# Kernel optimization log

Measured on AMD Instinct MI355X. Metric: run time of the kernel, lower is better.

Reference implementation:

```python
import jax, jax.numpy as jnp
import numpy as np

EPS = 1e-5  # torch LayerNorm default

def _ln(x, w, b):
    mu = jnp.mean(x, axis=-1, keepdims=True)
    var = jnp.mean((x - mu) ** 2, axis=-1, keepdims=True)
    return (x - mu) * jax.lax.rsqrt(var + EPS) * w + b

def setup_inputs() -> dict:
    B, C, P, D = 256, 256, 256, 256  # broadcasting in final add requires B==P==C
    key = jax.random.key(0)
    ks = jax.random.split(key, 10)
    d_rsqrt = D ** -0.5
    return {
        "x": jax.random.normal(ks[0], (B, C), dtype=jnp.float32),
        "prev_cell_out": jax.random.normal(ks[1], (P, D), dtype=jnp.float32),
        "feature_emb_weight": jax.random.uniform(ks[2], (C, D), minval=-d_rsqrt, maxval=d_rsqrt),
        "feature_emb_bias": jax.random.uniform(ks[3], (1, C, D), minval=-d_rsqrt, maxval=d_rsqrt),
        "ln_emb_w": jnp.ones((D,), jnp.float32), "ln_emb_b": jnp.zeros((D,), jnp.float32),
        "ln_col_w": jnp.ones((D,), jnp.float32), "ln_col_b": jnp.zeros((D,), jnp.float32),
        "ln_prompt_w": jnp.ones((D,), jnp.float32), "ln_prompt_b": jnp.zeros((D,), jnp.float32),
        "dense_imp_w": jax.random.normal(ks[4], (D, 2 * D)) * (2 * D) ** -0.5,  # torch Linear weight [out,in]
        "dense_imp_b": jnp.zeros((D,), jnp.float32),
        "emb_column": jax.random.normal(ks[5], (C, D)) * 0.01,
        "emb_prompt": jax.random.normal(ks[6], (P, D)) * 0.01,
        "expand_weight": jax.random.normal(ks[7], (P, 1)),  # dense_expand.weight [n_prompts, 1]
        "expand_bias": jax.random.normal(ks[8], (P,)) * 0.01,
    }

def reference(x, prev_cell_out, feature_emb_weight, feature_emb_bias,
              ln_emb_w, ln_emb_b, ln_col_w, ln_col_b, ln_prompt_w, ln_prompt_b,
              dense_imp_w, dense_imp_b, emb_column, emb_prompt,
              expand_weight, expand_bias):
    # addcmul: bias + x[...,None] * weight -> [B, C, D]
    x_emb = _ln(jax.nn.relu(feature_emb_bias + x[..., None] * feature_emb_weight), ln_emb_w, ln_emb_b)
    # prompt path (unbatched): [P, 2D] -> [P, D]
    xp_in = jnp.concatenate([_ln(emb_prompt, ln_prompt_w, ln_prompt_b), prev_cell_out], axis=-1)
    x_prompt = xp_in @ dense_imp_w.T + dense_imp_b + emb_prompt
    x_col = _ln(emb_column, ln_col_w, ln_col_b)  # [C, D]
    mask = jax.nn.softmax(x_prompt @ x_col.T, axis=-1)  # [P, C]
    # einsum 'pc,bcd->bpd'
    x_out = jnp.einsum('pc,bcd->bpd', mask, x_emb)
    # 'pc,bcd,pa->bpd' with a==1 is the same contraction scaled per-prompt by expand_weight[p,0]
    x_out = x_out * (1.0 + expand_weight[:, 0])[None, :, None]
    # 'pc,p->pc' then unsqueeze(0).unsqueeze(-1): [1, P, C, 1]; broadcasts [B,P,D] -> [1,B,P,D]
    bias_term = (mask * expand_bias[:, None])[None, :, :, None]
    return x_out + bias_term  # [1, B, P, D] (B==P==C)
```

## Files before the change

kernel.cpp:

```cpp
#include <hip/hip_runtime.h>
#include <cstdint>

typedef _Float16 half8 __attribute__((ext_vector_type(8)));
typedef float f32x4 __attribute__((ext_vector_type(4)));

#define LN_EPS 1e-5f

__device__ __forceinline__ float dot4(float4 a, float4 b) {
  return a.x*b.x + a.y*b.y + a.z*b.z + a.w*b.w;
}

__global__ __launch_bounds__(256) void k_pre(
    const float* __restrict__ x, const float* __restrict__ few, const float* __restrict__ feb,
    const float* __restrict__ emb_pr, const float* __restrict__ lnp_w, const float* __restrict__ lnp_b,
    const float* __restrict__ prev, const float* __restrict__ W, const float* __restrict__ Wb,
    const float* __restrict__ emb_col, const float* __restrict__ lnc_w, const float* __restrict__ lnc_b,
    float2* __restrict__ stats2, float* __restrict__ mask_f32, _Float16* __restrict__ mask_f16)
{
  __shared__ __align__(16) struct {
    float xin[512];
    float xq[256];
    float sc[256];
    float wr1[4], wr2[4];
  } sm;

  int t = threadIdx.x, w = t >> 6, lane = t & 63;

  if (blockIdx.x >= 256) {
    int bid = blockIdx.x - 256;
    int b = bid >> 3;
    int cg = (bid & 7) * 4 + w;
    int c0 = cg * 8;
    float xv[8];
    #pragma unroll
    for (int j = 0; j < 8; ++j) xv[j] = x[b*256 + c0 + j];
    float s1[8], s2[8];
    #pragma unroll
    for (int j = 0; j < 8; ++j) { s1[j] = 0.f; s2[j] = 0.f; }
    #pragma unroll
    for (int j = 0; j < 8; ++j) {
      float4 fw = ((const float4*)few)[(c0+j)*64 + lane];
      float4 fb = ((const float4*)feb)[(c0+j)*64 + lane];
      float4 v;
      v.x = fmaxf(fb.x + xv[j]*fw.x, 0.f);
      v.y = fmaxf(fb.y + xv[j]*fw.y, 0.f);
      v.z = fmaxf(fb.z + xv[j]*fw.z, 0.f);
      v.w = fmaxf(fb.w + xv[j]*fw.w, 0.f);
      s1[j] += v.x + v.y + v.z + v.w;
      s2[j] += v.x*v.x + v.y*v.y + v.z*v.z + v.w*v.w;
    }
    #pragma unroll
    for (int o = 32; o > 0; o >>= 1) {
      #pragma unroll
      for (int j = 0; j < 8; ++j) { s1[j] += __shfl_xor(s1[j], o); s2[j] += __shfl_xor(s2[j], o); }
    }
    float mu[8], rs[8];
    #pragma unroll
    for (int j = 0; j < 8; ++j) {
      mu[j] = s1[j] * (1.0f/256.0f);
      float var = s2[j] * (1.0f/256.0f) - mu[j]*mu[j];
      rs[j] = rsqrtf(var + LN_EPS);
    }
    float muv = mu[0], rsv = rs[0];
    #pragma unroll
    for (int j = 1; j < 8; ++j) {
      muv = (lane == j) ? mu[j] : muv;
      rsv = (lane == j) ? rs[j] : rsv;
    }
    if (lane < 8) stats2[b*256 + c0 + lane] = make_float2(muv, rsv);
    return;
  }

  int p = blockIdx.x;
  int q = t & 3, g = t >> 2;

  {
    float4 v = ((const float4*)emb_pr)[p*64 + lane];
    float s1 = v.x + v.y + v.z + v.w;
    float s2 = v.x*v.x + v.y*v.y + v.z*v.z + v.w*v.w;
    #pragma unroll
    for (int o = 32; o > 0; o >>= 1) { s1 += __shfl_xor(s1, o); s2 += __shfl_xor(s2, o); }
    float mu = s1 * (1.0f/256.0f);
    float var = s2 * (1.0f/256.0f) - mu*mu;
    float rsv = rsqrtf(var + LN_EPS);
    float4 w4 = ((const float4*)lnp_w)[lane];
    float4 b4 = ((const float4*)lnp_b)[lane];
    float4 y;
    y.x = (v.x-mu)*rsv*w4.x + b4.x;  y.y = (v.y-mu)*rsv*w4.y + b4.y;
    y.z = (v.z-mu)*rsv*w4.z + b4.z;  y.w = (v.w-mu)*rsv*w4.w + b4.w;
    if (w == 0) {
      ((float4*)sm.xin)[lane] = y;
      ((float4*)sm.xin)[64 + lane] = ((const float4*)prev)[p*64 + lane];
    }
  }
  __syncthreads();

  {
    float acc[4] = {0.f, 0.f, 0.f, 0.f};
    #pragma unroll 4
    for (int j = 0; j < 32; ++j) {
      int k4 = j*4 + q;
      float4 xv = ((const float4*)sm.xin)[k4];
      #pragma unroll
      for (int pp = 0; pp < 4; ++pp) {
        int d = pp*64 + g;
        float4 wv = ((const float4*)W)[d*128 + k4];
        acc[pp] += dot4(wv, xv);
      }
    }
    #pragma unroll
    for (int pp = 0; pp < 4; ++pp) {
      acc[pp] += __shfl_xor(acc[pp], 1);
      acc[pp] += __shfl_xor(acc[pp], 2);
    }
    if (q == 0) {
      #pragma unroll
      for (int pp = 0; pp < 4; ++pp) {
        int d = pp*64 + g;
        sm.xq[d] = acc[pp] + Wb[d] + emb_pr[p*256 + d];
      }
    }
  }
  __syncthreads();

  {
    float s1[4] = {0,0,0,0}, s2[4] = {0,0,0,0};
    #pragma unroll 4
    for (int j = 0; j < 16; ++j) {
      int k4 = j*4 + q;
      #pragma unroll
      for (int pp = 0; pp < 4; ++pp) {
        float4 v = ((const float4*)emb_col)[(pp*64+g)*64 + k4];
        s1[pp] += v.x + v.y + v.z + v.w;
        s2[pp] += v.x*v.x + v.y*v.y + v.z*v.z + v.w*v.w;
      }
    }
    float mu[4], rs[4];
    #pragma unroll
    for (int pp = 0; pp < 4; ++pp) {
      s1[pp] += __shfl_xor(s1[pp], 1);  s1[pp] += __shfl_xor(s1[pp], 2);
      s2[pp] += __shfl_xor(s2[pp], 1);  s2[pp] += __shfl_xor(s2[pp], 2);
      mu[pp] = s1[pp] * (1.0f/256.0f);
      float var = s2[pp] * (1.0f/256.0f) - mu[pp]*mu[pp];
      rs[pp] = rsqrtf(var + LN_EPS);
    }
    float acc[4] = {0.f, 0.f, 0.f, 0.f};
    #pragma unroll 4
    for (int j = 0; j < 16; ++j) {
      int k4 = j*4 + q;
      float4 lw4 = ((const float4*)lnc_w)[k4];
      float4 lb4 = ((const float4*)lnc_b)[k4];
      float4 xv = ((const float4*)sm.xq)[k4];
      #pragma unroll
      for (int pp = 0; pp < 4; ++pp) {
        float4 v = ((const float4*)emb_col)[(pp*64+g)*64 + k4];
        float4 nc;
        nc.x = (v.x-mu[pp])*rs[pp]*lw4.x + lb4.x;
        nc.y = (v.y-mu[pp])*rs[pp]*lw4.y + lb4.y;
        nc.z = (v.z-mu[pp])*rs[pp]*lw4.z + lb4.z;
        nc.w = (v.w-mu[pp])*rs[pp]*lw4.w + lb4.w;
        acc[pp] += dot4(nc, xv);
      }
    }
    #pragma unroll
    for (int pp = 0; pp < 4; ++pp) {
      acc[pp] += __shfl_xor(acc[pp], 1);
      acc[pp] += __shfl_xor(acc[pp], 2);
    }
    if (q == 0) {
      #pragma unroll
      for (int pp = 0; pp < 4; ++pp) sm.sc[pp*64 + g] = acc[pp];
    }
  }
  __syncthreads();

  {
    float val = sm.sc[t];
    float m0 = val;
    #pragma unroll
    for (int o = 32; o > 0; o >>= 1) m0 = fmaxf(m0, __shfl_xor(m0, o));
    if (lane == 0) sm.wr1[w] = m0;
    __syncthreads();
    float M = fmaxf(fmaxf(sm.wr1[0], sm.wr1[1]), fmaxf(sm.wr1[2], sm.wr1[3]));
    float e = expf(val - M);
    float s = e;
    #pragma unroll
    for (int o = 32; o > 0; o >>= 1) s += __shfl_xor(s, o);
    if (lane == 0) sm.wr2[w] = s;
    __syncthreads();
    float S = sm.wr2[0] + sm.wr2[1] + sm.wr2[2] + sm.wr2[3];
    float mv = e / S;
    mask_f32[p*256 + t] = mv;
    mask_f16[p*256 + t] = (_Float16)mv;
  }
}

__global__ __launch_bounds__(256) void k_main(
    const float* __restrict__ x, const float* __restrict__ few, const float* __restrict__ feb,
    const float* __restrict__ ln_emb_w, const float* __restrict__ ln_emb_b,
    const float2* __restrict__ stats2,
    const _Float16* __restrict__ mask_f16, const float* __restrict__ mask_f32,
    const float* __restrict__ ew, const float* __restrict__ eb,
    float* __restrict__ out)
{
  __shared__ __align__(16) _Float16 Bs[2][8 * 64 * 8];
  __shared__ float xrow[256];
  __shared__ __align__(8) float2 srow[256];

  const int t = threadIdx.x, w = t >> 6, lane = t & 63;
  const int lm = lane & 15, quad = lane >> 4;
  const int b  = blockIdx.x >> 2;
  const int ds = (blockIdx.x & 3) * 64;
  const int dl = t & 63;
  const int d  = ds + dl;

  half8 mf[2][4];
  #pragma unroll
  for (int ks = 0; ks < 2; ++ks)
    #pragma unroll
    for (int nt = 0; nt < 4; ++nt)
      mf[ks][nt] = *(const half8*)(mask_f16 + (size_t)(w*64 + nt*16 + lm)*256 + ks*32 + quad*8);

  xrow[t] = x[b*256 + t];
  srow[t] = stats2[b*256 + t];
  const float lwv = ln_emb_w[d];
  const float lbv = ln_emb_b[d];

  f32x4 acc[4][4];
  #pragma unroll
  for (int i = 0; i < 4; ++i)
    #pragma unroll
    for (int j = 0; j < 4; ++j)
      acc[i][j] = (f32x4){0.f, 0.f, 0.f, 0.f};

  float fwv[16], fbv[16];
  #pragma unroll
  for (int j = 0; j < 16; ++j) {
    int cl = w*16 + j;
    fwv[j] = few[cl*256 + d];
    fbv[j] = feb[cl*256 + d];
  }
  __syncthreads();
  {
    half8 h0, h1;
    #pragma unroll
    for (int j = 0; j < 16; ++j) {
      int cl = w*16 + j;
      float2 st = srow[cl];
      float v = fmaxf(fbv[j] + xrow[cl]*fwv[j], 0.f);
      _Float16 hh = (_Float16)((v - st.x) * st.y * lwv + lbv);
      if (j < 8) h0[j] = hh; else h1[j-8] = hh;
    }
    *(half8*)(&Bs[0][((w*2 + 0)*64 + dl)*8]) = h0;
    *(half8*)(&Bs[0][((w*2 + 1)*64 + dl)*8]) = h1;
  }
  __syncthreads();

  #pragma unroll
  for (int kb = 0; kb < 4; ++kb) {
    if (kb < 3) {
      #pragma unroll
      for (int j = 0; j < 16; ++j) {
        int cl = (kb+1)*64 + w*16 + j;
        fwv[j] = few[cl*256 + d];
        fbv[j] = feb[cl*256 + d];
      }
    }
    const _Float16* Bcur = &Bs[kb & 1][0];
    #pragma unroll
    for (int ks = 0; ks < 2; ++ks) {
      half8 xf[4];
      #pragma unroll
      for (int mt = 0; mt < 4; ++mt)
        xf[mt] = *(const half8*)(Bcur + ((ks*4 + quad)*64 + mt*16 + lm)*8);
      #pragma unroll
      for (int mt = 0; mt < 4; ++mt)
        #pragma unroll
        for (int nt = 0; nt < 4; ++nt)
          acc[mt][nt] = __builtin_amdgcn_mfma_f32_16x16x32_f16(xf[mt], mf[ks][nt], acc[mt][nt], 0, 0, 0);
    }
    if (kb < 3) {
      #pragma unroll
      for (int ks = 0; ks < 2; ++ks)
        #pragma unroll
        for (int nt = 0; nt < 4; ++nt)
          mf[ks][nt] = *(const half8*)(mask_f16 + (size_t)(w*64 + nt*16 + lm)*256 + (kb+1)*64 + ks*32 + quad*8);
      half8 h0, h1;
      #pragma unroll
      for (int j = 0; j < 16; ++j) {
        int cl = (kb+1)*64 + w*16 + j;
        float2 st = srow[cl];
        float v = fmaxf(fbv[j] + xrow[cl]*fwv[j], 0.f);
        _Float16 hh = (_Float16)((v - st.x) * st.y * lwv + lbv);
        if (j < 8) h0[j] = hh; else h1[j-8] = hh;
      }
      *(half8*)(&Bs[(kb+1) & 1][((w*2 + 0)*64 + dl)*8]) = h0;
      *(half8*)(&Bs[(kb+1) & 1][((w*2 + 1)*64 + dl)*8]) = h1;
      __syncthreads();
    }
  }

  const float ebv = eb[b];
  float sp[4], tb[4];
  #pragma unroll
  for (int nt = 0; nt < 4; ++nt) {
    int p = w*64 + nt*16 + lm;
    sp[nt] = 1.0f + ew[p];
    tb[nt] = mask_f32[b*256 + p] * ebv;
  }
  #pragma unroll
  for (int mt = 0; mt < 4; ++mt) {
    #pragma unroll
    for (int nt = 0; nt < 4; ++nt) {
      int p = w*64 + nt*16 + lm;
      int dd = ds + mt*16 + quad*4;
      f32x4 o = acc[mt][nt] * sp[nt] + tb[nt];
      *(f32x4*)(out + ((size_t)b << 16) + ((size_t)p << 8) + dd) = o;
    }
  }
}

extern "C" void kernel_launch(void* const* d_in, const int* in_sizes, int n_in,
                              void* d_out, int out_size, void* d_ws, size_t ws_size,
                              hipStream_t stream) {
  const float* x        = (const float*)d_in[0];
  const float* prev     = (const float*)d_in[1];
  const float* few      = (const float*)d_in[2];
  const float* feb      = (const float*)d_in[3];
  const float* ln_emb_w = (const float*)d_in[4];
  const float* ln_emb_b = (const float*)d_in[5];
  const float* ln_col_w = (const float*)d_in[6];
  const float* ln_col_b = (const float*)d_in[7];
  const float* ln_pr_w  = (const float*)d_in[8];
  const float* ln_pr_b  = (const float*)d_in[9];
  const float* dimp_w   = (const float*)d_in[10];
  const float* dimp_b   = (const float*)d_in[11];
  const float* emb_col  = (const float*)d_in[12];
  const float* emb_pr   = (const float*)d_in[13];
  const float* ew       = (const float*)d_in[14];
  const float* eb       = (const float*)d_in[15];
  float* out = (float*)d_out;

  char* wsb = (char*)d_ws;
  float2*   ws_stats  = (float2*)(wsb);
  float*    ws_mask   = (float*)(wsb + 524288);
  _Float16* ws_mask_h = (_Float16*)(wsb + 786432);

  k_pre<<<dim3(256 + 2048), dim3(256), 0, stream>>>(
      x, few, feb,
      emb_pr, ln_pr_w, ln_pr_b, prev, dimp_w, dimp_b,
      emb_col, ln_col_w, ln_col_b,
      ws_stats, ws_mask, ws_mask_h);
  k_main<<<dim3(1024), dim3(256), 0, stream>>>(
      x, few, feb, ln_emb_w, ln_emb_b,
      ws_stats, ws_mask_h, ws_mask, ew, eb, out);
}
```

Before: 148.1 us.

## Stage all embedding K-blocks in LDS upfront, then run MFMA with register-prefetched mask

The interleaved double-buffered pipeline is replaced by two phases. First, all four K-blocks of the LayerNorm'd embedding tile are computed and written to a larger LDS buffer behind a single barrier. Then the MFMA loop runs with no barriers, ping-ponging mask fragments between two register sets so the next block's mask load is issued before the current block's MFMAs. This removes three block-wide syncs, at the cost of more LDS (32KB for Bs), extra registers, and no overlap between the embedding compute and the MFMAs.

```diff
diff --git a/kernel.cpp b/kernel.cpp
--- a/kernel.cpp
+++ b/kernel.cpp
@@ -203,7 +203,7 @@
     const float* __restrict__ ew, const float* __restrict__ eb,
     float* __restrict__ out)
 {
-  __shared__ __align__(16) _Float16 Bs[2][8 * 64 * 8];
+  __shared__ __align__(16) _Float16 Bs[4 * 8 * 64 * 8];
   __shared__ float xrow[256];
   __shared__ __align__(8) float2 srow[256];
 
@@ -214,12 +214,12 @@
   const int dl = t & 63;
   const int d  = ds + dl;
 
-  half8 mf[2][4];
+  half8 mf0[2][4], mf1[2][4];
   #pragma unroll
   for (int ks = 0; ks < 2; ++ks)
     #pragma unroll
     for (int nt = 0; nt < 4; ++nt)
-      mf[ks][nt] = *(const half8*)(mask_f16 + (size_t)(w*64 + nt*16 + lm)*256 + ks*32 + quad*8);
+      mf0[ks][nt] = *(const half8*)(mask_f16 + (size_t)(w*64 + nt*16 + lm)*256 + ks*32 + quad*8);
 
   xrow[t] = x[b*256 + t];
   srow[t] = stats2[b*256 + t];
@@ -233,72 +233,55 @@
     for (int j = 0; j < 4; ++j)
       acc[i][j] = (f32x4){0.f, 0.f, 0.f, 0.f};
 
-  float fwv[16], fbv[16];
-  #pragma unroll
-  for (int j = 0; j < 16; ++j) {
-    int cl = w*16 + j;
-    fwv[j] = few[cl*256 + d];
-    fbv[j] = feb[cl*256 + d];
-  }
-  __syncthreads();
-  {
+  __syncthreads();
+
+  #pragma unroll
+  for (int kb = 0; kb < 4; ++kb) {
+    float fwv[16], fbv[16];
+    #pragma unroll
+    for (int j = 0; j < 16; ++j) {
+      int cl = kb*64 + w*16 + j;
+      fwv[j] = few[cl*256 + d];
+      fbv[j] = feb[cl*256 + d];
+    }
     half8 h0, h1;
     #pragma unroll
     for (int j = 0; j < 16; ++j) {
-      int cl = w*16 + j;
+      int cl = kb*64 + w*16 + j;
       float2 st = srow[cl];
       float v = fmaxf(fbv[j] + xrow[cl]*fwv[j], 0.f);
       _Float16 hh = (_Float16)((v - st.x) * st.y * lwv + lbv);
       if (j < 8) h0[j] = hh; else h1[j-8] = hh;
     }
-    *(half8*)(&Bs[0][((w*2 + 0)*64 + dl)*8]) = h0;
-    *(half8*)(&Bs[0][((w*2 + 1)*64 + dl)*8]) = h1;
-  }
-  __syncthreads();
-
-  #pragma unroll
-  for (int kb = 0; kb < 4; ++kb) {
-    if (kb < 3) {
-      #pragma unroll
-      for (int j = 0; j < 16; ++j) {
-        int cl = (kb+1)*64 + w*16 + j;
-        fwv[j] = few[cl*256 + d];
-        fbv[j] = feb[cl*256 + d];
-      }
-    }
-    const _Float16* Bcur = &Bs[kb & 1][0];
-    #pragma unroll
-    for (int ks = 0; ks < 2; ++ks) {
-      half8 xf[4];
-      #pragma unroll
-      for (int mt = 0; mt < 4; ++mt)
-        xf[mt] = *(const half8*)(Bcur + ((ks*4 + quad)*64 + mt*16 + lm)*8);
-      #pragma unroll
-      for (int mt = 0; mt < 4; ++mt)
-        #pragma unroll
-        for (int nt = 0; nt < 4; ++nt)
-          acc[mt][nt] = __builtin_amdgcn_mfma_f32_16x16x32_f16(xf[mt], mf[ks][nt], acc[mt][nt], 0, 0, 0);
-    }
-    if (kb < 3) {
-      #pragma unroll
-      for (int ks = 0; ks < 2; ++ks)
-        #pragma unroll
-        for (int nt = 0; nt < 4; ++nt)
-          mf[ks][nt] = *(const half8*)(mask_f16 + (size_t)(w*64 + nt*16 + lm)*256 + (kb+1)*64 + ks*32 + quad*8);
-      half8 h0, h1;
-      #pragma unroll
-      for (int j = 0; j < 16; ++j) {
-        int cl = (kb+1)*64 + w*16 + j;
-        float2 st = srow[cl];
-        float v = fmaxf(fbv[j] + xrow[cl]*fwv[j], 0.f);
-        _Float16 hh = (_Float16)((v - st.x) * st.y * lwv + lbv);
-        if (j < 8) h0[j] = hh; else h1[j-8] = hh;
-      }
-      *(half8*)(&Bs[(kb+1) & 1][((w*2 + 0)*64 + dl)*8]) = h0;
-      *(half8*)(&Bs[(kb+1) & 1][((w*2 + 1)*64 + dl)*8]) = h1;
-      __syncthreads();
-    }
-  }
+    *(half8*)(&Bs[((kb*8 + w*2 + 0)*64 + dl)*8]) = h0;
+    *(half8*)(&Bs[((kb*8 + w*2 + 1)*64 + dl)*8]) = h1;
+  }
+  __syncthreads();
+
+#define MFMA_KB(KB, MFC, MFN, DO_PRE)                                           \
+  {                                                                             \
+    if (DO_PRE) {                                                               \
+      _Pragma("unroll") for (int ks = 0; ks < 2; ++ks)                          \
+        _Pragma("unroll") for (int nt = 0; nt < 4; ++nt)                        \
+          MFN[ks][nt] = *(const half8*)(mask_f16 +                              \
+              (size_t)(w*64 + nt*16 + lm)*256 + ((KB)+1)*64 + ks*32 + quad*8);  \
+    }                                                                           \
+    _Pragma("unroll") for (int ks = 0; ks < 2; ++ks) {                          \
+      half8 xf[4];                                                              \
+      _Pragma("unroll") for (int mt = 0; mt < 4; ++mt)                          \
+        xf[mt] = *(const half8*)(&Bs[(((KB)*8 + ks*4 + quad)*64 + mt*16 + lm)*8]); \
+      _Pragma("unroll") for (int mt = 0; mt < 4; ++mt)                          \
+        _Pragma("unroll") for (int nt = 0; nt < 4; ++nt)                        \
+          acc[mt][nt] = __builtin_amdgcn_mfma_f32_16x16x32_f16(                 \
+              xf[mt], MFC[ks][nt], acc[mt][nt], 0, 0, 0);                       \
+    }                                                                           \
+  }
+
+  MFMA_KB(0, mf0, mf1, 1)
+  MFMA_KB(1, mf1, mf0, 1)
+  MFMA_KB(2, mf0, mf1, 1)
+  MFMA_KB(3, mf1, mf0, 0)
+#undef MFMA_KB
 
   const float ebv = eb[b];
   float sp[4], tb[4];
```

Result: no change. 146.6 us (median of 2 runs) (-1.0%).

## Process two batch rows per block to reuse mask fragments and embedding weights

Applied to the files above, without the earlier changes.

Each k_main block now handles two batch indices, so each mask fragment and feature weight load serves two MFMA accumulator sets, and the grid is halved. The x_emb tile is built for the whole K range in shared memory up front instead of a double-buffered pipeline, and output writes become nontemporal stores. This cuts redundant global loads of the mask and weights per output. In exchange it doubles accumulator registers and uses much more LDS, which lowers occupancy, and it gives up overlap between building the tile and running the MFMAs.

```diff
diff --git a/kernel.cpp b/kernel.cpp
--- a/kernel.cpp
+++ b/kernel.cpp
@@ -203,120 +203,123 @@
     const float* __restrict__ ew, const float* __restrict__ eb,
     float* __restrict__ out)
 {
-  __shared__ __align__(16) _Float16 Bs[2][8 * 64 * 8];
-  __shared__ float xrow[256];
-  __shared__ __align__(8) float2 srow[256];
+  __shared__ __align__(16) _Float16 Bs0[4 * 8 * 64 * 8];
+  __shared__ __align__(16) _Float16 Bs1[4 * 8 * 64 * 8];
+  __shared__ float xrow0[256], xrow1[256];
+  __shared__ __align__(8) float2 srow0[256], srow1[256];
 
   const int t = threadIdx.x, w = t >> 6, lane = t & 63;
   const int lm = lane & 15, quad = lane >> 4;
-  const int b  = blockIdx.x >> 2;
+  const int b0 = (blockIdx.x >> 2) << 1, b1 = b0 + 1;
   const int ds = (blockIdx.x & 3) * 64;
   const int dl = t & 63;
   const int d  = ds + dl;
 
-  half8 mf[2][4];
-  #pragma unroll
-  for (int ks = 0; ks < 2; ++ks)
-    #pragma unroll
-    for (int nt = 0; nt < 4; ++nt)
-      mf[ks][nt] = *(const half8*)(mask_f16 + (size_t)(w*64 + nt*16 + lm)*256 + ks*32 + quad*8);
-
-  xrow[t] = x[b*256 + t];
-  srow[t] = stats2[b*256 + t];
+  xrow0[t] = x[b0*256 + t];
+  xrow1[t] = x[b1*256 + t];
+  srow0[t] = stats2[b0*256 + t];
+  srow1[t] = stats2[b1*256 + t];
   const float lwv = ln_emb_w[d];
   const float lbv = ln_emb_b[d];
 
-  f32x4 acc[4][4];
+  f32x4 accA[4][4], accB[4][4];
   #pragma unroll
   for (int i = 0; i < 4; ++i)
     #pragma unroll
-    for (int j = 0; j < 4; ++j)
-      acc[i][j] = (f32x4){0.f, 0.f, 0.f, 0.f};
-
-  float fwv[16], fbv[16];
-  #pragma unroll
-  for (int j = 0; j < 16; ++j) {
-    int cl = w*16 + j;
-    fwv[j] = few[cl*256 + d];
-    fbv[j] = feb[cl*256 + d];
-  }
-  __syncthreads();
-  {
-    half8 h0, h1;
-    #pragma unroll
-    for (int j = 0; j < 16; ++j) {
-      int cl = w*16 + j;
-      float2 st = srow[cl];
-      float v = fmaxf(fbv[j] + xrow[cl]*fwv[j], 0.f);
-      _Float16 hh = (_Float16)((v - st.x) * st.y * lwv + lbv);
-      if (j < 8) h0[j] = hh; else h1[j-8] = hh;
-    }
-    *(half8*)(&Bs[0][((w*2 + 0)*64 + dl)*8]) = h0;
-    *(half8*)(&Bs[0][((w*2 + 1)*64 + dl)*8]) = h1;
-  }
+    for (int j = 0; j < 4; ++j) {
+      accA[i][j] = (f32x4){0.f, 0.f, 0.f, 0.f};
+      accB[i][j] = (f32x4){0.f, 0.f, 0.f, 0.f};
+    }
+
   __syncthreads();
 
   #pragma unroll
   for (int kb = 0; kb < 4; ++kb) {
-    if (kb < 3) {
-      #pragma unroll
-      for (int j = 0; j < 16; ++j) {
-        int cl = (kb+1)*64 + w*16 + j;
-        fwv[j] = few[cl*256 + d];
-        fbv[j] = feb[cl*256 + d];
-      }
-    }
-    const _Float16* Bcur = &Bs[kb & 1][0];
+    half8 hA0, hA1, hB0, hB1;
+    #pragma unroll
+    for (int j = 0; j < 16; ++j) {
+      int cl = kb*64 + w*16 + j;
+      float fw = few[cl*256 + d];
+      float fb = feb[cl*256 + d];
+      float2 s0 = srow0[cl];
+      float2 s1 = srow1[cl];
+      float v0 = fmaxf(fb + xrow0[cl]*fw, 0.f);
+      float v1 = fmaxf(fb + xrow1[cl]*fw, 0.f);
+      _Float16 h0 = (_Float16)((v0 - s0.x) * s0.y * lwv + lbv);
+      _Float16 h1 = (_Float16)((v1 - s1.x) * s1.y * lwv + lbv);
+      if (j < 8) { hA0[j] = h0; hB0[j] = h1; }
+      else       { hA1[j-8] = h0; hB1[j-8] = h1; }
+    }
+    *(half8*)(&Bs0[((kb*8 + w*2 + 0)*64 + dl)*8]) = hA0;
+    *(half8*)(&Bs0[((kb*8 + w*2 + 1)*64 + dl)*8]) = hA1;
+    *(half8*)(&Bs1[((kb*8 + w*2 + 0)*64 + dl)*8]) = hB0;
+    *(half8*)(&Bs1[((kb*8 + w*2 + 1)*64 + dl)*8]) = hB1;
+  }
+  __syncthreads();
+
+  #pragma unroll
+  for (int kb = 0; kb < 4; ++kb) {
+    half8 mf[2][4];
+    #pragma unroll
+    for (int ks = 0; ks < 2; ++ks)
+      #pragma unroll
+      for (int nt = 0; nt < 4; ++nt)
+        mf[ks][nt] = *(const half8*)(mask_f16 + (size_t)(w*64 + nt*16 + lm)*256 + kb*64 + ks*32 + quad*8);
     #pragma unroll
     for (int ks = 0; ks < 2; ++ks) {
-      half8 xf[4];
-      #pragma unroll
-      for (int mt = 0; mt < 4; ++mt)
-        xf[mt] = *(const half8*)(Bcur + ((ks*4 + quad)*64 + mt*16 + lm)*8);
+      half8 xf0[4], xf1[4];
+      #pragma unroll
+      for (int mt = 0; mt < 4; ++mt) {
+        xf0[mt] = *(const half8*)(&Bs0[((kb*8 + ks*4 + quad)*64 + mt*16 + lm)*8]);
+        xf1[mt] = *(const half8*)(&Bs1[((kb*8 + ks*4 + quad)*64 + mt*16 + lm)*8]);
+      }
       #pragma unroll
       for (int mt = 0; mt < 4; ++mt)
         #pragma unroll
-        for (int nt = 0; nt < 4; ++nt)
-          acc[mt][nt] = __builtin_amdgcn_mfma_f32_16x16x32_f16(xf[mt], mf[ks][nt], acc[mt][nt], 0, 0, 0);
-    }
-    if (kb < 3) {
-      #pragma unroll
-      for (int ks = 0; ks < 2; ++ks)
-        #pragma unroll
-        for (int nt = 0; nt < 4; ++nt)
-          mf[ks][nt] = *(const half8*)(mask_f16 + (size_t)(w*64 + nt*16 + lm)*256 + (kb+1)*64 + ks*32 + quad*8);
-      half8 h0, h1;
-      #pragma unroll
-      for (int j = 0; j < 16; ++j) {
-        int cl = (kb+1)*64 + w*16 + j;
-        float2 st = srow[cl];
-        float v = fmaxf(fbv[j] + xrow[cl]*fwv[j], 0.f);
-        _Float16 hh = (_Float16)((v - st.x) * st.y * lwv + lbv);
-        if (j < 8) h0[j] = hh; else h1[j-8] = hh;
-      }
-      *(half8*)(&Bs[(kb+1) & 1][((w*2 + 0)*64 + dl)*8]) = h0;
-      *(half8*)(&Bs[(kb+1) & 1][((w*2 + 1)*64 + dl)*8]) = h1;
-      __syncthreads();
-    }
-  }
-
-  const float ebv = eb[b];
-  float sp[4], tb[4];
-  #pragma unroll
-  for (int nt = 0; nt < 4; ++nt) {
-    int p = w*64 + nt*16 + lm;
-    sp[nt] = 1.0f + ew[p];
-    tb[nt] = mask_f32[b*256 + p] * ebv;
-  }
-  #pragma unroll
-  for (int mt = 0; mt < 4; ++mt) {
+        for (int nt = 0; nt < 4; ++nt) {
+          accA[mt][nt] = __builtin_amdgcn_mfma_f32_16x16x32_f16(xf0[mt], mf[ks][nt], accA[mt][nt], 0, 0, 0);
+          accB[mt][nt] = __builtin_amdgcn_mfma_f32_16x16x32_f16(xf1[mt], mf[ks][nt], accB[mt][nt], 0, 0, 0);
+        }
+    }
+  }
+
+  {
+    const float ebv = eb[b0];
+    float sp[4], tb[4];
     #pragma unroll
     for (int nt = 0; nt < 4; ++nt) {
       int p = w*64 + nt*16 + lm;
-      int dd = ds + mt*16 + quad*4;
-      f32x4 o = acc[mt][nt] * sp[nt] + tb[nt];
-      *(f32x4*)(out + ((size_t)b << 16) + ((size_t)p << 8) + dd) = o;
-    }
+      sp[nt] = 1.0f + ew[p];
+      tb[nt] = mask_f32[b0*256 + p] * ebv;
+    }
+    #pragma unroll
+    for (int mt = 0; mt < 4; ++mt)
+      #pragma unroll
+      for (int nt = 0; nt < 4; ++nt) {
+        int p = w*64 + nt*16 + lm;
+        int dd = ds + mt*16 + quad*4;
+        f32x4 o = accA[mt][nt] * sp[nt] + tb[nt];
+        __builtin_nontemporal_store(o, (f32x4*)(out + ((size_t)b0 << 16) + ((size_t)p << 8) + dd));
+      }
+  }
+  {
+    const float ebv = eb[b1];
+    float sp[4], tb[4];
+    #pragma unroll
+    for (int nt = 0; nt < 4; ++nt) {
+      int p = w*64 + nt*16 + lm;
+      sp[nt] = 1.0f + ew[p];
+      tb[nt] = mask_f32[b1*256 + p] * ebv;
+    }
+    #pragma unroll
+    for (int mt = 0; mt < 4; ++mt)
+      #pragma unroll
+      for (int nt = 0; nt < 4; ++nt) {
+        int p = w*64 + nt*16 + lm;
+        int dd = ds + mt*16 + quad*4;
+        f32x4 o = accB[mt][nt] * sp[nt] + tb[nt];
+        __builtin_nontemporal_store(o, (f32x4*)(out + ((size_t)b1 << 16) + ((size_t)p << 8) + dd));
+      }
   }
 }
 
@@ -351,7 +354,7 @@
       emb_pr, ln_pr_w, ln_pr_b, prev, dimp_w, dimp_b,
       emb_col, ln_col_w, ln_col_b,
       ws_stats, ws_mask, ws_mask_h);
-  k_main<<<dim3(1024), dim3(256), 0, stream>>>(
+  k_main<<<dim3(512), dim3(256), 0, stream>>>(
       x, few, feb, ln_emb_w, ln_emb_b,
       ws_stats, ws_mask_h, ws_mask, ew, eb, out);
 }
```

Result: slower. 154.7 us (+4.5%).
